# Optimization experiments

Hardware: AMD Instinct MI355X
Metric: run time of the kernel (lower is better)

The kernel has to match this reference:

```python
import jax, jax.numpy as jnp
import numpy as np

B, N, C = 2, 2048, 768
H = 12
HD = C // H  # 64
EPS = 1e-6


def setup_inputs() -> dict:
    key = jax.random.key(0)
    ks = jax.random.split(key, 6)
    x = jax.random.normal(ks[0], (B, N, C), dtype=jnp.float32)
    # Xavier-uniform-ish init for kernels
    lim_qkv = float(np.sqrt(6.0 / (C + 3 * C)))
    lim_proj = float(np.sqrt(6.0 / (C + C)))
    qkv_kernel = jax.random.uniform(ks[1], (C, 3 * C), minval=-lim_qkv, maxval=lim_qkv, dtype=jnp.float32)
    qkv_bias = jnp.zeros((3 * C,), dtype=jnp.float32)
    proj_kernel = jax.random.uniform(ks[2], (C, C), minval=-lim_proj, maxval=lim_proj, dtype=jnp.float32)
    proj_bias = jnp.zeros((C,), dtype=jnp.float32)
    q_norm_w = jnp.ones((HD,), dtype=jnp.float32)
    k_norm_w = jnp.ones((HD,), dtype=jnp.float32)
    # Standard RoPE tables: freqs over half the head dim, tiled to full head_dim
    half = HD // 2
    inv_freq = 1.0 / (10000.0 ** (jnp.arange(0, half, dtype=jnp.float32) / half))
    t = jnp.arange(N, dtype=jnp.float32)
    freqs = jnp.outer(t, inv_freq)               # (N, HD/2)
    emb = jnp.concatenate([freqs, freqs], axis=-1)  # (N, HD)
    rope_cos = jnp.cos(emb)
    rope_sin = jnp.sin(emb)
    return {"x": x, "rope_cos": rope_cos, "rope_sin": rope_sin,
            "qkv_kernel": qkv_kernel, "qkv_bias": qkv_bias,
            "proj_kernel": proj_kernel, "proj_bias": proj_bias,
            "q_norm_w": q_norm_w, "k_norm_w": k_norm_w}


def _rms_norm(x, w):
    var = jnp.mean(x * x, axis=-1, keepdims=True)
    return x * jax.lax.rsqrt(var + EPS) * w


def _rope(x, cos, sin):
    # x: (B, H, N, HD); cos/sin: (N, HD)
    half = x.shape[-1] // 2
    x1, x2 = x[..., :half], x[..., half:]
    rot = jnp.concatenate([-x2, x1], axis=-1)
    return x * cos + rot * sin


def reference(x, rope_cos, rope_sin, qkv_kernel, qkv_bias, proj_kernel, proj_bias, q_norm_w, k_norm_w):
    b, n, c = x.shape
    qkv = x @ qkv_kernel + qkv_bias                       # (B, N, 3C)
    qkv = qkv.reshape(b, n, 3, H, HD).transpose(2, 0, 3, 1, 4)  # (3, B, H, N, HD)
    q, k, v = qkv[0], qkv[1], qkv[2]
    q = _rope(_rms_norm(q, q_norm_w), rope_cos, rope_sin)
    k = _rope(_rms_norm(k, k_norm_w), rope_cos, rope_sin)
    scale = 1.0 / jnp.sqrt(jnp.float32(HD)).astype(x.dtype)
    attn = jnp.einsum('bhqd,bhkd->bhqk', q, k) * scale    # (B, H, N, N)
    attn = jax.nn.softmax(attn, axis=-1)
    out = jnp.einsum('bhqk,bhkd->bhqd', attn, v)          # (B, H, N, HD)
    out = out.swapaxes(1, 2).reshape(b, n, c)
    return out @ proj_kernel + proj_bias
```

## Files before the change

kernel.cpp:

```cpp
#include <hip/hip_runtime.h>
#include <math.h>

#define B_    2
#define N_    2048
#define C_    768
#define H_    12
#define HD_   64
#define NROWS (B_*N_)
#define QKVC  (3*C_)
#define EPSV  1e-6f
#define SCALE 0.125f
#define LOG2E 1.44269504088896f
#define SMAX  12.0f

typedef unsigned short u16;
typedef short bf16x8 __attribute__((ext_vector_type(8)));
typedef float f32x4  __attribute__((ext_vector_type(4)));

__device__ __forceinline__ float b2f(u16 u) {
    unsigned v = ((unsigned)u) << 16;
    return __builtin_bit_cast(float, v);
}
__device__ __forceinline__ u16 f2b(float f) {
    unsigned u = __builtin_bit_cast(unsigned, f);
    u += 0x7fffu + ((u >> 16) & 1u);
    return (u16)(u >> 16);
}
__device__ __forceinline__ unsigned pk2(float a, float b) {
#if __has_builtin(__builtin_amdgcn_cvt_pk_bf16_f32)
    auto r = __builtin_amdgcn_cvt_pk_bf16_f32(a, b);
    return __builtin_bit_cast(unsigned, r);
#else
    return (unsigned)f2b(a) | ((unsigned)f2b(b) << 16);
#endif
}
__device__ __forceinline__ float fexp2(float x) {
#if __has_builtin(__builtin_amdgcn_exp2f)
    return __builtin_amdgcn_exp2f(x);
#else
    return exp2f(x);
#endif
}
__device__ __forceinline__ void gload_lds16(const void* g, void* l) {
    __builtin_amdgcn_global_load_lds(
        (const __attribute__((address_space(1))) unsigned int*)g,
        (__attribute__((address_space(3))) unsigned int*)l, 16, 0, 0);
}

__global__ __launch_bounds__(256)
void prep_kernel(const float* __restrict__ x,
                 const float* __restrict__ qkv_w,
                 const float* __restrict__ proj_w,
                 u16* __restrict__ xb,
                 u16* __restrict__ qwt,
                 u16* __restrict__ pwt) {
    __shared__ float T[64][65];
    const int t = threadIdx.x;
    if (blockIdx.x < 3072) {
        const int i = (blockIdx.x * 256 + t) * 4;
        const float4 v = *(const float4*)(x + i);
        uint2 o = { pk2(v.x, v.y), pk2(v.z, v.w) };
        *(uint2*)(xb + i) = o;
        return;
    }
    const float* W; u16* Wt; int K, N, k0, n0;
    if (blockIdx.x < 3072 + 432) {
        const int bx = blockIdx.x - 3072;
        W = qkv_w; Wt = qwt; K = C_; N = QKVC;
        n0 = (bx % 36) * 64; k0 = (bx / 36) * 64;
    } else {
        const int bx = blockIdx.x - 3504;
        W = proj_w; Wt = pwt; K = C_; N = C_;
        n0 = (bx % 12) * 64; k0 = (bx / 12) * 64;
    }
    const int r = t >> 6, c = t & 63;
#pragma unroll
    for (int p = 0; p < 16; ++p) {
        const int kl = p * 4 + r;
        T[kl][c] = W[(size_t)(k0 + kl) * N + n0 + c];
    }
    __syncthreads();
#pragma unroll
    for (int p = 0; p < 16; ++p) {
        const int nl = p * 4 + r;
        Wt[(size_t)(n0 + nl) * K + k0 + c] = f2b(T[c][nl]);
    }
}

template <bool BF16OUT>
__global__ __launch_bounds__(256)
void gemm_tn_kernel(const u16* __restrict__ A, const u16* __restrict__ Bt,
                    const float* __restrict__ bias, void* __restrict__ Cout,
                    int M, int N, int K) {
    __shared__ __attribute__((aligned(16))) u16 As[128 * 32];
    __shared__ __attribute__((aligned(16))) u16 Bs[128 * 32];
    const int tid = threadIdx.x;
    const int w = tid >> 6, l = tid & 63;
    const int lq = l & 15, quad = l >> 4;
    const int mbase = blockIdx.y * 128, nbase = blockIdx.x * 128;

    f32x4 acc[4][4];
    const f32x4 z4 = {0.f, 0.f, 0.f, 0.f};
#pragma unroll
    for (int mb = 0; mb < 4; ++mb)
#pragma unroll
        for (int nb = 0; nb < 4; ++nb) acc[mb][nb] = z4;

    const int srow = (l >> 2);
    const int sdc  = (l & 3) ^ ((l >> 2) & 3);

    for (int k0 = 0; k0 < K; k0 += 32) {
#pragma unroll
        for (int cc = 0; cc < 2; ++cc) {
            const int c = 2 * w + cc;
            const int row = 16 * c + srow;
            gload_lds16(A  + (size_t)(mbase + row) * K + k0 + sdc * 8, &As[c * 512]);
            gload_lds16(Bt + (size_t)(nbase + row) * K + k0 + sdc * 8, &Bs[c * 512]);
        }
        __syncthreads();

        bf16x8 af[4], bfr[4];
#pragma unroll
        for (int mb = 0; mb < 4; ++mb)
            af[mb] = *(const bf16x8*)
                &As[((w >> 1) * 64 + mb * 16 + lq) * 32 + ((quad ^ (lq & 3)) * 8)];
#pragma unroll
        for (int nb = 0; nb < 4; ++nb)
            bfr[nb] = *(const bf16x8*)
                &Bs[((w & 1) * 64 + nb * 16 + lq) * 32 + ((quad ^ (lq & 3)) * 8)];
#pragma unroll
        for (int mb = 0; mb < 4; ++mb)
#pragma unroll
            for (int nb = 0; nb < 4; ++nb)
                acc[mb][nb] = __builtin_amdgcn_mfma_f32_16x16x32_bf16(
                    af[mb], bfr[nb], acc[mb][nb], 0, 0, 0);
        __syncthreads();
    }

#pragma unroll
    for (int nb = 0; nb < 4; ++nb) {
        const int col = nbase + (w & 1) * 64 + nb * 16 + lq;
        const float bv = bias[col];
#pragma unroll
        for (int mb = 0; mb < 4; ++mb) {
#pragma unroll
            for (int r = 0; r < 4; ++r) {
                const int row = mbase + (w >> 1) * 64 + mb * 16 + quad * 4 + r;
                const float v = acc[mb][nb][r] + bv;
                if (BF16OUT) ((u16*)Cout)[(size_t)row * N + col] = f2b(v);
                else         ((float*)Cout)[(size_t)row * N + col] = v;
            }
        }
    }
}

__global__ __launch_bounds__(64)
void gemm_tn64_kernel(const u16* __restrict__ A, const u16* __restrict__ Bt,
                      const float* __restrict__ bias, float* __restrict__ Cout,
                      int M, int N, int K) {
    __shared__ __attribute__((aligned(16))) u16 As[64 * 32];
    __shared__ __attribute__((aligned(16))) u16 Bs[64 * 32];
    const int l = threadIdx.x;
    const int lq = l & 15, quad = l >> 4;
    const int mbase = blockIdx.y * 64, nbase = blockIdx.x * 64;

    f32x4 acc[4][4];
    const f32x4 z4 = {0.f, 0.f, 0.f, 0.f};
#pragma unroll
    for (int mb = 0; mb < 4; ++mb)
#pragma unroll
        for (int nb = 0; nb < 4; ++nb) acc[mb][nb] = z4;

    const int srow = (l >> 2);
    const int sdc  = (l & 3) ^ ((l >> 2) & 3);

    for (int k0 = 0; k0 < K; k0 += 32) {
#pragma unroll
        for (int c = 0; c < 4; ++c) {
            const int row = 16 * c + srow;
            gload_lds16(A  + (size_t)(mbase + row) * K + k0 + sdc * 8, &As[c * 512]);
            gload_lds16(Bt + (size_t)(nbase + row) * K + k0 + sdc * 8, &Bs[c * 512]);
        }
        __syncthreads();

        bf16x8 af[4], bfr[4];
#pragma unroll
        for (int mb = 0; mb < 4; ++mb)
            af[mb] = *(const bf16x8*)
                &As[(mb * 16 + lq) * 32 + ((quad ^ (lq & 3)) * 8)];
#pragma unroll
        for (int nb = 0; nb < 4; ++nb)
            bfr[nb] = *(const bf16x8*)
                &Bs[(nb * 16 + lq) * 32 + ((quad ^ (lq & 3)) * 8)];
#pragma unroll
        for (int mb = 0; mb < 4; ++mb)
#pragma unroll
            for (int nb = 0; nb < 4; ++nb)
                acc[mb][nb] = __builtin_amdgcn_mfma_f32_16x16x32_bf16(
                    af[mb], bfr[nb], acc[mb][nb], 0, 0, 0);
        __syncthreads();
    }

#pragma unroll
    for (int nb = 0; nb < 4; ++nb) {
        const int col = nbase + nb * 16 + lq;
        const float bv = bias[col];
#pragma unroll
        for (int mb = 0; mb < 4; ++mb) {
#pragma unroll
            for (int r = 0; r < 4; ++r) {
                const int row = mbase + mb * 16 + quad * 4 + r;
                Cout[(size_t)row * N + col] = acc[mb][nb][r] + bv;
            }
        }
    }
}

__global__ __launch_bounds__(256)
void normrope_kernel(u16* __restrict__ qkv,
                     const float* __restrict__ cosb,
                     const float* __restrict__ sinb,
                     const float* __restrict__ qw,
                     const float* __restrict__ kw) {
    const int item = blockIdx.x * 16 + (threadIdx.x >> 4);
    const int lq   = threadIdx.x & 15;
    const int h    = item % H_;
    const int row  = item / H_;
    const int n    = row & (N_ - 1);
    const size_t base = (size_t)row * QKVC + h * HD_ + lq * 4;

    const ushort4 q4 = *(const ushort4*)&qkv[base];
    const ushort4 k4 = *(const ushort4*)&qkv[base + C_];
    float qf[4], kf[4];
    qf[0] = b2f(q4.x); qf[1] = b2f(q4.y); qf[2] = b2f(q4.z); qf[3] = b2f(q4.w);
    kf[0] = b2f(k4.x); kf[1] = b2f(k4.y); kf[2] = b2f(k4.z); kf[3] = b2f(k4.w);

    float q2 = qf[0]*qf[0] + qf[1]*qf[1] + qf[2]*qf[2] + qf[3]*qf[3];
    float k2 = kf[0]*kf[0] + kf[1]*kf[1] + kf[2]*kf[2] + kf[3]*kf[3];
#pragma unroll
    for (int off = 8; off >= 1; off >>= 1) {
        q2 += __shfl_xor(q2, off, 64);
        k2 += __shfl_xor(k2, off, 64);
    }
    const float rq = rsqrtf(q2 * (1.f / 64.f) + EPSV);
    const float rk = rsqrtf(k2 * (1.f / 64.f) + EPSV);

    const float4 qwv = *(const float4*)&qw[lq * 4];
    const float4 kwv = *(const float4*)&kw[lq * 4];
    const float4 cv  = *(const float4*)&cosb[n * HD_ + lq * 4];
    const float4 sv  = *(const float4*)&sinb[n * HD_ + lq * 4];

    float qn[4], kn[4];
    qn[0] = qf[0]*rq*qwv.x; qn[1] = qf[1]*rq*qwv.y;
    qn[2] = qf[2]*rq*qwv.z; qn[3] = qf[3]*rq*qwv.w;
    kn[0] = kf[0]*rk*kwv.x; kn[1] = kf[1]*rk*kwv.y;
    kn[2] = kf[2]*rk*kwv.z; kn[3] = kf[3]*rk*kwv.w;

    const float sgn = (lq < 8) ? -1.f : 1.f;
    float qo[4], ko[4];
    const float cc[4] = {cv.x, cv.y, cv.z, cv.w};
    const float ss[4] = {sv.x, sv.y, sv.z, sv.w};
#pragma unroll
    for (int j = 0; j < 4; ++j) {
        const float qp = __shfl_xor(qn[j], 8, 64);
        const float kp = __shfl_xor(kn[j], 8, 64);
        qo[j] = (qn[j] * cc[j] + sgn * qp * ss[j]) * (SCALE * LOG2E);
        ko[j] =  kn[j] * cc[j] + sgn * kp * ss[j];
    }
    uint2 qout = { pk2(qo[0], qo[1]), pk2(qo[2], qo[3]) };
    uint2 kout = { pk2(ko[0], ko[1]), pk2(ko[2], ko[3]) };
    *(uint2*)&qkv[base]      = qout;
    *(uint2*)&qkv[base + C_] = kout;
}

__global__ __launch_bounds__(256)
void kvpack_kernel(const u16* __restrict__ qkv,
                   u16* __restrict__ kpack, u16* __restrict__ vpack) {
    __shared__ u16 Tk[64][72];
    __shared__ u16 Tv[64][72];
    const int kt = blockIdx.x & 31, bh = blockIdx.x >> 5;
    const int b = bh / H_, h = bh % H_;
    const int t = threadIdx.x;
    {
        const int r = t >> 2, seg = t & 3;
        const u16* srck = &qkv[(size_t)(b * N_ + kt * 64 + r) * QKVC
                               + C_ + h * HD_ + seg * 16];
        *(uint4*)&Tk[r][seg * 16]     = *(const uint4*)srck;
        *(uint4*)&Tk[r][seg * 16 + 8] = *(const uint4*)(srck + 8);
        const u16* srcv = srck + C_;
        *(uint4*)&Tv[r][seg * 16]     = *(const uint4*)srcv;
        *(uint4*)&Tv[r][seg * 16 + 8] = *(const uint4*)(srcv + 8);
    }
    __syncthreads();
    const size_t tile = ((size_t)bh * 32 + kt) * 4096;
    u16 ktmp[16], vtmp[16];
#pragma unroll
    for (int g2 = 0; g2 < 2; ++g2) {
        const int g = t * 2 + g2;
        const int blk = g >> 6;
        const int l  = g & 63;
        const int bb = blk >> 1, ks = blk & 1;
        const int m  = l & 15,  quad = l >> 4;
#pragma unroll
        for (int j = 0; j < 8; ++j) {
            ktmp[g2 * 8 + j] = Tk[bb * 16 + m][ks * 32 + quad * 8 + j];
            vtmp[g2 * 8 + j] = Tv[ks * 32 + quad * 8 + j][bb * 16 + m];
        }
    }
    u16* kd = &kpack[tile + t * 16];
    *(uint4*)kd       = *(const uint4*)&ktmp[0];
    *(uint4*)(kd + 8) = *(const uint4*)&ktmp[8];
    u16* vd = &vpack[tile + t * 16];
    *(uint4*)vd       = *(const uint4*)&vtmp[0];
    *(uint4*)(vd + 8) = *(const uint4*)&vtmp[8];
}

__global__ __launch_bounds__(128, 2)
void flash_mfma_kernel(const u16* __restrict__ qkv,
                       const u16* __restrict__ kpack,
                       const u16* __restrict__ vpack,
                       u16* __restrict__ opart,
                       float* __restrict__ lpart) {
    __shared__ __attribute__((aligned(16))) u16 Ps[2][64 * 64];
    __shared__ float lex[64];
    float* Oex = (float*)&Ps[0][0];

    const int tid = threadIdx.x;
    const int w = tid >> 6, l = tid & 63;
    const int lq = l & 15, quad = l >> 4;
    const int sw = lq & 7;

    const int lin  = blockIdx.x;
    const int slot = lin >> 3;
    const int bh   = (lin & 7) * 3 + (slot >> 6);
    const int rem  = slot & 63;
    const int qt   = rem >> 1;
    const int kh   = rem & 1;
    const int b = bh / H_, h = bh % H_;
    const size_t qbase = (size_t)b * N_ * QKVC + h * HD_;
    const size_t tbase = (size_t)bh * 32 * 4096;

    bf16x8 onesf;
    {
        const short one = (short)0x3F80;
        const short v = (lq == 0) ? one : (short)0;
#pragma unroll
        for (int j = 0; j < 8; ++j) onesf[j] = v;
    }

    bf16x8 qb[4][2];
#pragma unroll
    for (int nq = 0; nq < 4; ++nq)
#pragma unroll
        for (int ks = 0; ks < 2; ++ks)
            qb[nq][ks] = *(const bf16x8*)
                &qkv[qbase + (size_t)(qt * 64 + nq * 16 + lq) * QKVC
                     + ks * 32 + quad * 8];

    f32x4 oacc[4][4], lacc[4];
    const f32x4 z4 = {0.f, 0.f, 0.f, 0.f};
#pragma unroll
    for (int mb = 0; mb < 4; ++mb)
#pragma unroll
        for (int nq = 0; nq < 4; ++nq) oacc[mb][nq] = z4;
#pragma unroll
    for (int nq = 0; nq < 4; ++nq) lacc[nq] = z4;

    bf16x8 ka[4][2];
#pragma unroll
    for (int kb = 0; kb < 4; ++kb)
#pragma unroll
        for (int ks = 0; ks < 2; ++ks)
            ka[kb][ks] = *(const bf16x8*)
                &kpack[tbase + (size_t)(kh * 16 + w) * 4096
                       + ((kb * 2 + ks) * 64 + l) * 8];

    for (int kt2 = 0; kt2 < 8; ++kt2) {
        const int kt  = kh * 16 + 2 * kt2 + w;
        const int ktn = kh * 16 + ((2 * kt2 + 2 + w) & 15);
        const size_t vb   = tbase + (size_t)kt * 4096;
        const size_t kb_n = tbase + (size_t)ktn * 4096;

        bf16x8 va[4][2];
#pragma unroll
        for (int mb = 0; mb < 4; ++mb)
#pragma unroll
            for (int ks = 0; ks < 2; ++ks)
                va[mb][ks] = *(const bf16x8*)
                    &vpack[vb + ((mb * 2 + ks) * 64 + l) * 8];

#pragma unroll
        for (int kb = 0; kb < 4; ++kb) {
            f32x4 sacc[4];
#pragma unroll
            for (int nq = 0; nq < 4; ++nq) sacc[nq] = z4;
#pragma unroll
            for (int ks = 0; ks < 2; ++ks)
#pragma unroll
                for (int nq = 0; nq < 4; ++nq)
                    sacc[nq] = __builtin_amdgcn_mfma_f32_16x16x32_bf16(
                        ka[kb][ks], qb[nq][ks], sacc[nq], 0, 0, 0);
#pragma unroll
            for (int nq = 0; nq < 4; ++nq) {
                float p[4];
#pragma unroll
                for (int r = 0; r < 4; ++r) p[r] = fexp2(sacc[nq][r] - SMAX);
                uint2 pkv = { pk2(p[0], p[1]), pk2(p[2], p[3]) };
                *(uint2*)&Ps[w][(nq * 16 + lq) * 64
                                + (((kb * 2 + (quad >> 1)) ^ sw) * 8)
                                + (quad & 1) * 4] = pkv;
            }
        }

#pragma unroll
        for (int kb = 0; kb < 4; ++kb)
#pragma unroll
            for (int ks = 0; ks < 2; ++ks)
                ka[kb][ks] = *(const bf16x8*)
                    &kpack[kb_n + ((kb * 2 + ks) * 64 + l) * 8];

        bf16x8 pb[2][4];
#pragma unroll
        for (int ks = 0; ks < 2; ++ks)
#pragma unroll
            for (int nq = 0; nq < 4; ++nq)
                pb[ks][nq] = *(const bf16x8*)
                    &Ps[w][(nq * 16 + lq) * 64 + (((ks * 4 + quad) ^ sw) * 8)];

#pragma unroll
        for (int mb = 0; mb < 4; ++mb)
#pragma unroll
            for (int ks = 0; ks < 2; ++ks)
#pragma unroll
                for (int nq = 0; nq < 4; ++nq)
                    oacc[mb][nq] = __builtin_amdgcn_mfma_f32_16x16x32_bf16(
                        va[mb][ks], pb[ks][nq], oacc[mb][nq], 0, 0, 0);
#pragma unroll
        for (int ks = 0; ks < 2; ++ks)
#pragma unroll
            for (int nq = 0; nq < 4; ++nq)
                lacc[nq] = __builtin_amdgcn_mfma_f32_16x16x32_bf16(
                    onesf, pb[ks][nq], lacc[nq], 0, 0, 0);
    }


    __syncthreads();
    if (w == 1) {
#pragma unroll
        for (int nq = 0; nq < 4; ++nq) {
#pragma unroll
            for (int mb = 0; mb < 4; ++mb) {
                const int chunkS = (mb * 4 + quad) ^ lq;
                float4 v;
                v.x = oacc[mb][nq][0]; v.y = oacc[mb][nq][1];
                v.z = oacc[mb][nq][2]; v.w = oacc[mb][nq][3];
                *(float4*)&Oex[(nq * 16 + lq) * 64 + chunkS * 4] = v;
            }
            if (quad == 0) lex[nq * 16 + lq] = lacc[nq][0];
        }
    }
    __syncthreads();
    if (w == 0) {
#pragma unroll
        for (int nq = 0; nq < 4; ++nq) {
#pragma unroll
            for (int mb = 0; mb < 4; ++mb) {
                const int chunkS = (mb * 4 + quad) ^ lq;
                float4* p = (float4*)&Oex[(nq * 16 + lq) * 64 + chunkS * 4];
                float4 v = *p;
                v.x += oacc[mb][nq][0]; v.y += oacc[mb][nq][1];
                v.z += oacc[mb][nq][2]; v.w += oacc[mb][nq][3];
                *p = v;
            }
            if (quad == 0) lex[nq * 16 + lq] += lacc[nq][0];
        }
    }
    __syncthreads();

    const size_t pbase_o = ((size_t)(bh * 32 + qt) * 2 + kh) * 4096;
    const size_t pbase_l = ((size_t)(bh * 32 + qt) * 2 + kh) * 64;
#pragma unroll
    for (int pass = 0; pass < 8; ++pass) {
        const int row = pass * 8 + (tid >> 4);
        const int c   = tid & 15;
        const int phys = c ^ (row & 15);
        const float4 v = *(const float4*)&Oex[row * 64 + phys * 4];
        uint2 o2 = { pk2(v.x, v.y), pk2(v.z, v.w) };
        *(uint2*)&opart[pbase_o + row * 64 + c * 4] = o2;
    }
    if (tid < 64) lpart[pbase_l + tid] = lex[tid];
}

__global__ __launch_bounds__(256)
void combine_kernel(const u16* __restrict__ opart,
                    const float* __restrict__ lpart,
                    u16* __restrict__ attnb) {
    const int lin  = blockIdx.x;
    const int slot = lin >> 3;
    const int bh   = (lin & 7) * 3 + (slot >> 5);
    const int qt   = slot & 31;
    const int b = bh / H_, h = bh % H_;
    const int t = threadIdx.x;
    const int q = t >> 2, g = t & 3;

    const size_t pair = (size_t)(bh * 32 + qt) * 2;
    const float lv = lpart[pair * 64 + q] + lpart[(pair + 1) * 64 + q];
    const float inv = 1.f / lv;

    const size_t p0 = pair * 4096 + q * 64 + g * 16;
    const size_t p1 = p0 + 4096;

    u16 res[16];
#pragma unroll
    for (int j4 = 0; j4 < 4; ++j4) {
        const ushort4 a = *(const ushort4*)&opart[p0 + j4 * 4];
        const ushort4 c = *(const ushort4*)&opart[p1 + j4 * 4];
        const float v0 = (b2f(a.x) + b2f(c.x)) * inv;
        const float v1 = (b2f(a.y) + b2f(c.y)) * inv;
        const float v2 = (b2f(a.z) + b2f(c.z)) * inv;
        const float v3 = (b2f(a.w) + b2f(c.w)) * inv;
        uint2 o2 = { pk2(v0, v1), pk2(v2, v3) };
        *(uint2*)&res[j4 * 4] = o2;
    }
    u16* dst = &attnb[(size_t)(b * N_ + qt * 64 + q) * C_ + h * HD_ + g * 16];
    *(uint4*)dst       = *(const uint4*)&res[0];
    *(uint4*)(dst + 8) = *(const uint4*)&res[8];
}

extern "C" void kernel_launch(void* const* d_in, const int* in_sizes, int n_in,
                              void* d_out, int out_size, void* d_ws, size_t ws_size,
                              hipStream_t stream) {
    const float* x        = (const float*)d_in[0];
    const float* rope_cos = (const float*)d_in[1];
    const float* rope_sin = (const float*)d_in[2];
    const float* qkv_w    = (const float*)d_in[3];
    const float* qkv_b    = (const float*)d_in[4];
    const float* proj_w   = (const float*)d_in[5];
    const float* proj_b   = (const float*)d_in[6];
    const float* q_nw     = (const float*)d_in[7];
    const float* k_nw     = (const float*)d_in[8];
    float* out = (float*)d_out;

    u16* xb     = (u16*)d_ws;
    u16* qwt    = xb     + (size_t)NROWS * C_;
    u16* pwt    = qwt    + (size_t)QKVC * C_;
    u16* qkvb   = pwt    + (size_t)C_ * C_;
    u16* vpackb = qkvb   + (size_t)NROWS * QKVC;
    u16* attnb  = vpackb + (size_t)B_ * H_ * 32 * 4096;
    u16* opartb = attnb  + (size_t)NROWS * C_;
    float* lpartb = (float*)(opartb + (size_t)1536 * 4096);
    u16* kpackb = xb;

    prep_kernel<<<dim3(3072 + 432 + 144), 256, 0, stream>>>(
        x, qkv_w, proj_w, xb, qwt, pwt);

    gemm_tn_kernel<true><<<dim3(QKVC / 128, NROWS / 128), 256, 0, stream>>>(
        xb, qwt, qkv_b, qkvb, NROWS, QKVC, C_);

    normrope_kernel<<<dim3(3072), 256, 0, stream>>>(
        qkvb, rope_cos, rope_sin, q_nw, k_nw);

    kvpack_kernel<<<dim3(768), 256, 0, stream>>>(qkvb, kpackb, vpackb);

    flash_mfma_kernel<<<dim3(1536), 128, 0, stream>>>(
        qkvb, kpackb, vpackb, opartb, lpartb);

    combine_kernel<<<dim3(768), 256, 0, stream>>>(opartb, lpartb, attnb);

    gemm_tn64_kernel<<<dim3(C_ / 64, NROWS / 64), 64, 0, stream>>>(
        attnb, pwt, proj_b, out, NROWS, C_, C_);
}
```

Baseline: 208.9 us.

## Split flash attention into single-wave blocks over 32-query tiles

Each flash-attention block becomes a single 64-thread wave handling 32 queries over half of the key range, replacing the two-wave 64-query block that reduced partial outputs through shared memory. The row sums are now accumulated with VALU adds plus lane shuffles instead of an extra MFMA against a ones vector. V fragments are double-buffered per mb rather than all loaded up front. This removes the intra-block reduction and barriers and doubles the grid, but each K/V tile is now loaded by twice as many blocks, which raises global/L2 traffic, and the combine kernel indexing is changed to match.

```diff
diff --git a/kernel.cpp b/kernel.cpp
--- a/kernel.cpp
+++ b/kernel.cpp
@@ -315,180 +315,142 @@
     *(uint4*)(vd + 8) = *(const uint4*)&vtmp[8];
 }
 
-__global__ __launch_bounds__(128, 2)
+__global__ __launch_bounds__(64, 3)
 void flash_mfma_kernel(const u16* __restrict__ qkv,
                        const u16* __restrict__ kpack,
                        const u16* __restrict__ vpack,
                        u16* __restrict__ opart,
                        float* __restrict__ lpart) {
-    __shared__ __attribute__((aligned(16))) u16 Ps[2][64 * 64];
-    __shared__ float lex[64];
-    float* Oex = (float*)&Ps[0][0];
-
-    const int tid = threadIdx.x;
-    const int w = tid >> 6, l = tid & 63;
+    __shared__ __attribute__((aligned(16))) u16 Ps[32 * 64];
+
+    const int l = threadIdx.x;
     const int lq = l & 15, quad = l >> 4;
     const int sw = lq & 7;
 
     const int lin  = blockIdx.x;
     const int slot = lin >> 3;
-    const int bh   = (lin & 7) * 3 + (slot >> 6);
-    const int rem  = slot & 63;
+    const int bh   = (lin & 7) * 3 + (slot >> 7);
+    const int rem  = slot & 127;
     const int qt   = rem >> 1;
     const int kh   = rem & 1;
     const int b = bh / H_, h = bh % H_;
     const size_t qbase = (size_t)b * N_ * QKVC + h * HD_;
     const size_t tbase = (size_t)bh * 32 * 4096;
 
-    bf16x8 onesf;
-    {
-        const short one = (short)0x3F80;
-        const short v = (lq == 0) ? one : (short)0;
-#pragma unroll
-        for (int j = 0; j < 8; ++j) onesf[j] = v;
-    }
-
-    bf16x8 qb[4][2];
-#pragma unroll
-    for (int nq = 0; nq < 4; ++nq)
+    bf16x8 qb[2][2];
+#pragma unroll
+    for (int nq = 0; nq < 2; ++nq)
 #pragma unroll
         for (int ks = 0; ks < 2; ++ks)
             qb[nq][ks] = *(const bf16x8*)
-                &qkv[qbase + (size_t)(qt * 64 + nq * 16 + lq) * QKVC
+                &qkv[qbase + (size_t)(qt * 32 + nq * 16 + lq) * QKVC
                      + ks * 32 + quad * 8];
 
-    f32x4 oacc[4][4], lacc[4];
+    float lsum[2] = {0.f, 0.f};
+    f32x4 oacc[4][2];
     const f32x4 z4 = {0.f, 0.f, 0.f, 0.f};
 #pragma unroll
     for (int mb = 0; mb < 4; ++mb)
 #pragma unroll
-        for (int nq = 0; nq < 4; ++nq) oacc[mb][nq] = z4;
-#pragma unroll
-    for (int nq = 0; nq < 4; ++nq) lacc[nq] = z4;
-
-    bf16x8 ka[4][2];
-#pragma unroll
-    for (int kb = 0; kb < 4; ++kb)
-#pragma unroll
-        for (int ks = 0; ks < 2; ++ks)
-            ka[kb][ks] = *(const bf16x8*)
-                &kpack[tbase + (size_t)(kh * 16 + w) * 4096
-                       + ((kb * 2 + ks) * 64 + l) * 8];
-
-    for (int kt2 = 0; kt2 < 8; ++kt2) {
-        const int kt  = kh * 16 + 2 * kt2 + w;
-        const int ktn = kh * 16 + ((2 * kt2 + 2 + w) & 15);
-        const size_t vb   = tbase + (size_t)kt * 4096;
-        const size_t kb_n = tbase + (size_t)ktn * 4096;
-
-        bf16x8 va[4][2];
-#pragma unroll
-        for (int mb = 0; mb < 4; ++mb)
+        for (int nq = 0; nq < 2; ++nq) oacc[mb][nq] = z4;
+
+    for (int kt2 = 0; kt2 < 16; ++kt2) {
+        const size_t ktile = tbase + (size_t)(kh * 16 + kt2) * 4096;
+
+        bf16x8 ka[4][2];
+#pragma unroll
+        for (int kb = 0; kb < 4; ++kb)
 #pragma unroll
             for (int ks = 0; ks < 2; ++ks)
-                va[mb][ks] = *(const bf16x8*)
-                    &vpack[vb + ((mb * 2 + ks) * 64 + l) * 8];
+                ka[kb][ks] = *(const bf16x8*)
+                    &kpack[ktile + ((kb * 2 + ks) * 64 + l) * 8];
 
 #pragma unroll
         for (int kb = 0; kb < 4; ++kb) {
-            f32x4 sacc[4];
-#pragma unroll
-            for (int nq = 0; nq < 4; ++nq) sacc[nq] = z4;
+            f32x4 sacc[2];
+#pragma unroll
+            for (int nq = 0; nq < 2; ++nq) sacc[nq] = z4;
 #pragma unroll
             for (int ks = 0; ks < 2; ++ks)
 #pragma unroll
-                for (int nq = 0; nq < 4; ++nq)
+                for (int nq = 0; nq < 2; ++nq)
                     sacc[nq] = __builtin_amdgcn_mfma_f32_16x16x32_bf16(
                         ka[kb][ks], qb[nq][ks], sacc[nq], 0, 0, 0);
 #pragma unroll
-            for (int nq = 0; nq < 4; ++nq) {
+            for (int nq = 0; nq < 2; ++nq) {
                 float p[4];
 #pragma unroll
                 for (int r = 0; r < 4; ++r) p[r] = fexp2(sacc[nq][r] - SMAX);
+                lsum[nq] += (p[0] + p[1]) + (p[2] + p[3]);
                 uint2 pkv = { pk2(p[0], p[1]), pk2(p[2], p[3]) };
-                *(uint2*)&Ps[w][(nq * 16 + lq) * 64
-                                + (((kb * 2 + (quad >> 1)) ^ sw) * 8)
-                                + (quad & 1) * 4] = pkv;
+                *(uint2*)&Ps[(nq * 16 + lq) * 64
+                             + (((kb * 2 + (quad >> 1)) ^ sw) * 8)
+                             + (quad & 1) * 4] = pkv;
             }
         }
 
-#pragma unroll
-        for (int kb = 0; kb < 4; ++kb)
+        bf16x8 pb[2][2];
+#pragma unroll
+        for (int ks = 0; ks < 2; ++ks)
+#pragma unroll
+            for (int nq = 0; nq < 2; ++nq)
+                pb[ks][nq] = *(const bf16x8*)
+                    &Ps[(nq * 16 + lq) * 64 + (((ks * 4 + quad) ^ sw) * 8)];
+
+        const size_t vtile = ktile;
+        bf16x8 vaA[2], vaB[2];
+#pragma unroll
+        for (int ks = 0; ks < 2; ++ks)
+            vaA[ks] = *(const bf16x8*)&vpack[vtile + ((ks) * 64 + l) * 8];
+#pragma unroll
+        for (int mb = 0; mb < 4; ++mb) {
+            if (mb < 3) {
+#pragma unroll
+                for (int ks = 0; ks < 2; ++ks)
+                    vaB[ks] = *(const bf16x8*)
+                        &vpack[vtile + (((mb + 1) * 2 + ks) * 64 + l) * 8];
+            }
 #pragma unroll
             for (int ks = 0; ks < 2; ++ks)
-                ka[kb][ks] = *(const bf16x8*)
-                    &kpack[kb_n + ((kb * 2 + ks) * 64 + l) * 8];
-
-        bf16x8 pb[2][4];
-#pragma unroll
-        for (int ks = 0; ks < 2; ++ks)
-#pragma unroll
-            for (int nq = 0; nq < 4; ++nq)
-                pb[ks][nq] = *(const bf16x8*)
-                    &Ps[w][(nq * 16 + lq) * 64 + (((ks * 4 + quad) ^ sw) * 8)];
-
-#pragma unroll
-        for (int mb = 0; mb < 4; ++mb)
-#pragma unroll
-            for (int ks = 0; ks < 2; ++ks)
-#pragma unroll
-                for (int nq = 0; nq < 4; ++nq)
+#pragma unroll
+                for (int nq = 0; nq < 2; ++nq)
                     oacc[mb][nq] = __builtin_amdgcn_mfma_f32_16x16x32_bf16(
-                        va[mb][ks], pb[ks][nq], oacc[mb][nq], 0, 0, 0);
-#pragma unroll
-        for (int ks = 0; ks < 2; ++ks)
-#pragma unroll
-            for (int nq = 0; nq < 4; ++nq)
-                lacc[nq] = __builtin_amdgcn_mfma_f32_16x16x32_bf16(
-                    onesf, pb[ks][nq], lacc[nq], 0, 0, 0);
-    }
-
-
-    __syncthreads();
-    if (w == 1) {
-#pragma unroll
-        for (int nq = 0; nq < 4; ++nq) {
-#pragma unroll
-            for (int mb = 0; mb < 4; ++mb) {
-                const int chunkS = (mb * 4 + quad) ^ lq;
-                float4 v;
-                v.x = oacc[mb][nq][0]; v.y = oacc[mb][nq][1];
-                v.z = oacc[mb][nq][2]; v.w = oacc[mb][nq][3];
-                *(float4*)&Oex[(nq * 16 + lq) * 64 + chunkS * 4] = v;
-            }
-            if (quad == 0) lex[nq * 16 + lq] = lacc[nq][0];
-        }
-    }
-    __syncthreads();
-    if (w == 0) {
-#pragma unroll
-        for (int nq = 0; nq < 4; ++nq) {
-#pragma unroll
-            for (int mb = 0; mb < 4; ++mb) {
-                const int chunkS = (mb * 4 + quad) ^ lq;
-                float4* p = (float4*)&Oex[(nq * 16 + lq) * 64 + chunkS * 4];
-                float4 v = *p;
-                v.x += oacc[mb][nq][0]; v.y += oacc[mb][nq][1];
-                v.z += oacc[mb][nq][2]; v.w += oacc[mb][nq][3];
-                *p = v;
-            }
-            if (quad == 0) lex[nq * 16 + lq] += lacc[nq][0];
-        }
-    }
-    __syncthreads();
-
-    const size_t pbase_o = ((size_t)(bh * 32 + qt) * 2 + kh) * 4096;
-    const size_t pbase_l = ((size_t)(bh * 32 + qt) * 2 + kh) * 64;
-#pragma unroll
-    for (int pass = 0; pass < 8; ++pass) {
-        const int row = pass * 8 + (tid >> 4);
-        const int c   = tid & 15;
-        const int phys = c ^ (row & 15);
-        const float4 v = *(const float4*)&Oex[row * 64 + phys * 4];
-        uint2 o2 = { pk2(v.x, v.y), pk2(v.z, v.w) };
-        *(uint2*)&opart[pbase_o + row * 64 + c * 4] = o2;
-    }
-    if (tid < 64) lpart[pbase_l + tid] = lex[tid];
+                        vaA[ks], pb[ks][nq], oacc[mb][nq], 0, 0, 0);
+#pragma unroll
+            for (int ks = 0; ks < 2; ++ks) vaA[ks] = vaB[ks];
+        }
+    }
+
+#pragma unroll
+    for (int nq = 0; nq < 2; ++nq) {
+        lsum[nq] += __shfl_xor(lsum[nq], 16, 64);
+        lsum[nq] += __shfl_xor(lsum[nq], 32, 64);
+    }
+
+#pragma unroll
+    for (int nq = 0; nq < 2; ++nq) {
+#pragma unroll
+        for (int mb = 0; mb < 4; ++mb) {
+            uint2 ov = { pk2(oacc[mb][nq][0], oacc[mb][nq][1]),
+                         pk2(oacc[mb][nq][2], oacc[mb][nq][3]) };
+            *(uint2*)&Ps[(nq * 16 + lq) * 64
+                         + (((mb * 2 + (quad >> 1)) ^ sw) * 8)
+                         + (quad & 1) * 4] = ov;
+        }
+    }
+    const size_t pbase_o = ((size_t)(bh * 64 + qt) * 2 + kh) * 2048;
+    const size_t pbase_l = ((size_t)(bh * 64 + qt) * 2 + kh) * 32;
+#pragma unroll
+    for (int pass = 0; pass < 4; ++pass) {
+        const int ql = pass * 8 + (l >> 3);
+        const int c  = l & 7;
+        const bf16x8 v = *(const bf16x8*)&Ps[ql * 64 + ((c ^ (ql & 7)) * 8)];
+        *(bf16x8*)&opart[pbase_o + ql * 64 + c * 8] = v;
+    }
+    if (quad == 0) {
+        lpart[pbase_l + lq]      = lsum[0];
+        lpart[pbase_l + 16 + lq] = lsum[1];
+    }
 }
 
 __global__ __launch_bounds__(256)
@@ -503,18 +465,21 @@
     const int t = threadIdx.x;
     const int q = t >> 2, g = t & 3;
 
-    const size_t pair = (size_t)(bh * 32 + qt) * 2;
-    const float lv = lpart[pair * 64 + q] + lpart[(pair + 1) * 64 + q];
+    const int tile32 = qt * 2 + (q >> 5);
+    const int r32    = q & 31;
+    const size_t p0  = ((size_t)(bh * 64 + tile32) * 2);
+
+    const float lv = lpart[p0 * 32 + r32] + lpart[p0 * 32 + 32 + r32];
     const float inv = 1.f / lv;
 
-    const size_t p0 = pair * 4096 + q * 64 + g * 16;
-    const size_t p1 = p0 + 4096;
+    const size_t o0 = p0 * 2048 + r32 * 64 + g * 16;
+    const size_t o1 = o0 + 2048;
 
     u16 res[16];
 #pragma unroll
     for (int j4 = 0; j4 < 4; ++j4) {
-        const ushort4 a = *(const ushort4*)&opart[p0 + j4 * 4];
-        const ushort4 c = *(const ushort4*)&opart[p1 + j4 * 4];
+        const ushort4 a = *(const ushort4*)&opart[o0 + j4 * 4];
+        const ushort4 c = *(const ushort4*)&opart[o1 + j4 * 4];
         const float v0 = (b2f(a.x) + b2f(c.x)) * inv;
         const float v1 = (b2f(a.y) + b2f(c.y)) * inv;
         const float v2 = (b2f(a.z) + b2f(c.z)) * inv;
@@ -548,7 +513,7 @@
     u16* vpackb = qkvb   + (size_t)NROWS * QKVC;
     u16* attnb  = vpackb + (size_t)B_ * H_ * 32 * 4096;
     u16* opartb = attnb  + (size_t)NROWS * C_;
-    float* lpartb = (float*)(opartb + (size_t)1536 * 4096);
+    float* lpartb = (float*)(opartb + (size_t)6144 * 2048);
     u16* kpackb = xb;
 
     prep_kernel<<<dim3(3072 + 432 + 144), 256, 0, stream>>>(
@@ -562,7 +527,7 @@
 
     kvpack_kernel<<<dim3(768), 256, 0, stream>>>(qkvb, kpackb, vpackb);
 
-    flash_mfma_kernel<<<dim3(1536), 128, 0, stream>>>(
+    flash_mfma_kernel<<<dim3(3072), 64, 0, stream>>>(
         qkvb, kpackb, vpackb, opartb, lpartb);
 
     combine_kernel<<<dim3(768), 256, 0, stream>>>(opartb, lpartb, attnb);
```

New measurement: 199.3 us. -4.6%, faster.
